# Kernel tuning notes

Hardware: AMD Instinct MI355X
Metric: run time of the kernel (lower is better)

Reference implementation:

```python
import jax, jax.numpy as jnp
import numpy as np

D_MODEL = 1024
D_KEY = 64
BATCH = 4
SEQ = 4096


def setup_inputs() -> dict:
    key = jax.random.key(0)
    kq, kk, kv, kwq, kwk, kwv = jax.random.split(key, 6)
    queries = jax.random.normal(kq, (BATCH, SEQ, D_MODEL), dtype=jnp.float32)
    keys = jax.random.normal(kk, (BATCH, SEQ, D_MODEL), dtype=jnp.float32)
    values = jax.random.normal(kv, (BATCH, SEQ, D_MODEL), dtype=jnp.float32)
    # causal mask: 1 = keep, 0 = masked out (torch masked_fill where mask==0)
    mask = jnp.tril(jnp.ones((SEQ, SEQ), dtype=jnp.int32))
    s = 1.0 / np.sqrt(D_MODEL)
    Wq = jax.random.normal(kwq, (D_MODEL, D_KEY), dtype=jnp.float32) * s
    Wk = jax.random.normal(kwk, (D_MODEL, D_KEY), dtype=jnp.float32) * s
    Wv = jax.random.normal(kwv, (D_MODEL, D_KEY), dtype=jnp.float32) * s
    return {"queries": queries, "keys": keys, "values": values,
            "mask": mask, "Wq": Wq, "Wk": Wk, "Wv": Wv}


def reference(queries, keys, values, mask, Wq, Wk, Wv):
    q = jnp.einsum('bsd,dk->bsk', queries, Wq)   # [B,S,dk]
    k = jnp.einsum('bsd,dk->bsk', keys, Wk)
    v = jnp.einsum('bsd,dk->bsk', values, Wv)
    scale = 1.0 / np.sqrt(D_KEY).astype(np.float32)
    attn = jnp.einsum('bqk,bsk->bqs', q, k) * scale  # [B,Sq,Sk]
    attn = jnp.where(mask == 0, -jnp.inf, attn)
    attn = jax.nn.softmax(attn, axis=-1)
    return jnp.einsum('bqs,bsk->bqk', attn, v)      # [B,S,dk]
```

## Files before the change

kernel.cpp:

```cpp
#include <hip/hip_runtime.h>
#include <hip/hip_bf16.h>

#define B      4
#define SEQ    4096
#define DM     1024
#define DK     64
#define NSPLIT 8

typedef __bf16 bf16x8 __attribute__((ext_vector_type(8)));
typedef __bf16 bf16x4 __attribute__((ext_vector_type(4)));
typedef float  f32x4  __attribute__((ext_vector_type(4)));

#define KSTR 72

#define QSCALE 0.1803368801111204f
#define M2BIAS 12.0f

__global__ __launch_bounds__(256) void wt_kernel(
    const float* __restrict__ Wq, const float* __restrict__ Wk,
    const float* __restrict__ Wv, __bf16* __restrict__ Wt)
{
    const int mat = blockIdx.y;
    const float* W = (mat == 0) ? Wq : (mat == 1) ? Wk : Wv;
    const float scale = (mat == 0) ? QSCALE : 1.0f;
    const int k0 = blockIdx.x * 64;
    const int tid = threadIdx.x;

    __shared__ float t[64][65];

    const int r = tid >> 2;
    const int c = (tid & 3) * 16;
    {
        const float* src = W + (size_t)(k0 + r) * DK + c;
        #pragma unroll
        for (int j = 0; j < 4; ++j) {
            float4 a = *(const float4*)(src + j * 4);
            t[r][c + j * 4 + 0] = a.x; t[r][c + j * 4 + 1] = a.y;
            t[r][c + j * 4 + 2] = a.z; t[r][c + j * 4 + 3] = a.w;
        }
    }
    __syncthreads();
    const int n  = tid >> 2;
    const int kk = (tid & 3) * 16;
    bf16x8 b0, b1;
    #pragma unroll
    for (int j = 0; j < 8; ++j) b0[j] = (__bf16)(t[kk + j][n] * scale);
    #pragma unroll
    for (int j = 0; j < 8; ++j) b1[j] = (__bf16)(t[kk + 8 + j][n] * scale);
    __bf16* dst = Wt + (size_t)(mat * DK + n) * DM + k0 + kk;
    *(bf16x8*)(dst)     = b0;
    *(bf16x8*)(dst + 8) = b1;
}

#define DA 8
#define DW 4
__global__ __launch_bounds__(256) void proj_stream_kernel(
    const float* __restrict__ q_in, const float* __restrict__ k_in,
    const float* __restrict__ v_in, const __bf16* __restrict__ Wt,
    __bf16* __restrict__ qb, __bf16* __restrict__ kb,
    __bf16* __restrict__ vtb)
{
    const int m = blockIdx.y;
    const float* in = (m == 0) ? q_in : (m == 1) ? k_in : v_in;
    const __bf16* wt = Wt + (size_t)m * DK * DM;

    const int rowbase = blockIdx.x * 64;
    const int tid  = threadIdx.x;
    const int w    = tid >> 6;
    const int lane = tid & 63;
    const int quad = lane >> 4;
    const int l15  = lane & 15;

    const float*  arow = in + (size_t)(rowbase + w * 16 + l15) * DM + quad * 8;
    const __bf16* wrow = wt + (size_t)l15 * DM + quad * 8;

    float4 Aa[DA], Ab[DA];
    bf16x8 Wb[DW][4];
    #pragma unroll
    for (int d = 0; d < DA; ++d) {
        const float* ap = arow + d * 32;
        Aa[d] = *(const float4*)(ap);
        Ab[d] = *(const float4*)(ap + 4);
    }
    #pragma unroll
    for (int d = 0; d < DW; ++d) {
        const __bf16* wp = wrow + d * 32;
        Wb[d][0] = *(const bf16x8*)(wp);
        Wb[d][1] = *(const bf16x8*)(wp + 16 * DM);
        Wb[d][2] = *(const bf16x8*)(wp + 32 * DM);
        Wb[d][3] = *(const bf16x8*)(wp + 48 * DM);
    }

    f32x4 acc[4];
    #pragma unroll
    for (int nf = 0; nf < 4; ++nf) acc[nf] = (f32x4){0.f, 0.f, 0.f, 0.f};

    #pragma unroll
    for (int it = 0; it < 32; ++it) {
        const int da = it & (DA - 1);
        const int dw = it & (DW - 1);
        bf16x8 af;
        af[0] = (__bf16)Aa[da].x; af[1] = (__bf16)Aa[da].y;
        af[2] = (__bf16)Aa[da].z; af[3] = (__bf16)Aa[da].w;
        af[4] = (__bf16)Ab[da].x; af[5] = (__bf16)Ab[da].y;
        af[6] = (__bf16)Ab[da].z; af[7] = (__bf16)Ab[da].w;
        acc[0] = __builtin_amdgcn_mfma_f32_16x16x32_bf16(af, Wb[dw][0], acc[0], 0, 0, 0);
        acc[1] = __builtin_amdgcn_mfma_f32_16x16x32_bf16(af, Wb[dw][1], acc[1], 0, 0, 0);
        acc[2] = __builtin_amdgcn_mfma_f32_16x16x32_bf16(af, Wb[dw][2], acc[2], 0, 0, 0);
        acc[3] = __builtin_amdgcn_mfma_f32_16x16x32_bf16(af, Wb[dw][3], acc[3], 0, 0, 0);
        if (it + DA < 32) {
            const float* ap = arow + (it + DA) * 32;
            Aa[da] = *(const float4*)(ap);
            Ab[da] = *(const float4*)(ap + 4);
        }
        if (it + DW < 32) {
            const __bf16* wp = wrow + (it + DW) * 32;
            Wb[dw][0] = *(const bf16x8*)(wp);
            Wb[dw][1] = *(const bf16x8*)(wp + 16 * DM);
            Wb[dw][2] = *(const bf16x8*)(wp + 32 * DM);
            Wb[dw][3] = *(const bf16x8*)(wp + 48 * DM);
        }
    }

    if (m < 2) {
        __bf16* outb = (m == 0) ? qb : kb;
        #pragma unroll
        for (int nf = 0; nf < 4; ++nf)
            #pragma unroll
            for (int r = 0; r < 4; ++r)
                outb[(size_t)(rowbase + w * 16 + quad * 4 + r) * DK + nf * 16 + l15] =
                    (__bf16)acc[nf][r];
    } else {
        const int bb = rowbase >> 12;
        const int s0 = (rowbase & (SEQ - 1)) + w * 16 + quad * 4;
        #pragma unroll
        for (int nf = 0; nf < 4; ++nf) {
            bf16x4 v4;
            #pragma unroll
            for (int r = 0; r < 4; ++r) v4[r] = (__bf16)acc[nf][r];
            *(bf16x4*)&vtb[(size_t)(bb * DK + nf * 16 + l15) * SEQ + s0] = v4;
        }
    }
}

__global__ __launch_bounds__(256) void flash_kernel(
    const __bf16* __restrict__ qb, const __bf16* __restrict__ kb,
    const __bf16* __restrict__ vtb, __bf16* __restrict__ Opart,
    float* __restrict__ lpart)
{
    const int qt  = blockIdx.x;
    const int bb  = blockIdx.y;
    const int z   = blockIdx.z;
    const int tid = threadIdx.x;
    const int w    = tid >> 6;
    const int lane = tid & 63;
    const int quad = lane >> 4;
    const int l15  = lane & 15;

    __shared__ __bf16 Ks[64 * KSTR];
    __shared__ __bf16 Vs[64 * KSTR];
    __shared__ __bf16 Ps[4][2][16 * KSTR];

    const int qrow_base = qt * 128 + w * 32;
    const int niters = 2 * qt + 2;
    const int kt0 = (niters * z) / NSPLIT;
    const int kt1 = (niters * (z + 1)) / NSPLIT;

    bf16x8 qf[2][2];
    #pragma unroll
    for (int g = 0; g < 2; ++g) {
        const __bf16* qp = qb + ((size_t)(bb * SEQ + qrow_base + g * 16 + l15)) * DK + quad * 8;
        qf[g][0] = *(const bf16x8*)(qp);
        qf[g][1] = *(const bf16x8*)(qp + 32);
    }

    bf16x8 ones;
    #pragma unroll
    for (int j = 0; j < 8; ++j) ones[j] = (__bf16)1.0f;

    f32x4 of[2][4], lacc[2];
    #pragma unroll
    for (int g = 0; g < 2; ++g) {
        #pragma unroll
        for (int nf = 0; nf < 4; ++nf) of[g][nf] = (f32x4){0.f, 0.f, 0.f, 0.f};
        lacc[g] = (f32x4){0.f, 0.f, 0.f, 0.f};
    }

    const int sr = tid >> 2;
    const int sc = (tid & 3) * 16;
    bf16x8 kr0, kr1, vr0, vr1;
    const __bf16* kbase = kb  + ((size_t)(bb * SEQ + sr)) * DK + sc;
    const __bf16* vbase = vtb + ((size_t)(bb * DK  + sr)) * SEQ + sc;

    if (kt1 > kt0) {
        const __bf16* kg = kbase + (size_t)kt0 * 64 * DK;
        kr0 = *(const bf16x8*)(kg); kr1 = *(const bf16x8*)(kg + 8);
        const __bf16* vg = vbase + kt0 * 64;
        vr0 = *(const bf16x8*)(vg); vr1 = *(const bf16x8*)(vg + 8);
    }

    for (int kt = kt0; kt < kt1; ++kt) {
        __syncthreads();
        *(bf16x8*)&Ks[sr * KSTR + sc]     = kr0;
        *(bf16x8*)&Ks[sr * KSTR + sc + 8] = kr1;
        *(bf16x8*)&Vs[sr * KSTR + sc]     = vr0;
        *(bf16x8*)&Vs[sr * KSTR + sc + 8] = vr1;
        __syncthreads();
        if (kt + 1 < kt1) {
            const __bf16* kg = kbase + (size_t)(kt + 1) * 64 * DK;
            kr0 = *(const bf16x8*)(kg); kr1 = *(const bf16x8*)(kg + 8);
            const __bf16* vg = vbase + (kt + 1) * 64;
            vr0 = *(const bf16x8*)(vg); vr1 = *(const bf16x8*)(vg + 8);
        }

        f32x4 sf[2][4];
        #pragma unroll
        for (int g = 0; g < 2; ++g)
            #pragma unroll
            for (int nf = 0; nf < 4; ++nf)
                sf[g][nf] = (f32x4){-M2BIAS, -M2BIAS, -M2BIAS, -M2BIAS};
        #pragma unroll
        for (int nf = 0; nf < 4; ++nf) {
            #pragma unroll
            for (int ch = 0; ch < 2; ++ch) {
                bf16x8 kf = *(const bf16x8*)(&Ks[(nf * 16 + l15) * KSTR + ch * 32 + quad * 8]);
                sf[0][nf] = __builtin_amdgcn_mfma_f32_16x16x32_bf16(qf[0][ch], kf, sf[0][nf], 0, 0, 0);
                sf[1][nf] = __builtin_amdgcn_mfma_f32_16x16x32_bf16(qf[1][ch], kf, sf[1][nf], 0, 0, 0);
            }
        }

        const int kc0 = kt * 64;
        #pragma unroll
        for (int g = 0; g < 2; ++g) {
            const int r0 = qrow_base + g * 16;
            const bool dg = (kc0 + 63 > r0);
            #pragma unroll
            for (int nf = 0; nf < 4; ++nf) {
                #pragma unroll
                for (int r = 0; r < 4; ++r) {
                    float s = sf[g][nf][r];
                    if (dg) {
                        const int col = kc0 + nf * 16 + l15;
                        const int row = r0 + quad * 4 + r;
                        if (col > row) s = -1.0e9f;
                    }
                    const float p = __builtin_amdgcn_exp2f(s);
                    Ps[w][g][(quad * 4 + r) * KSTR + nf * 16 + l15] = (__bf16)p;
                }
            }
        }

        bf16x8 pf[2][2];
        #pragma unroll
        for (int g = 0; g < 2; ++g) {
            pf[g][0] = *(const bf16x8*)(&Ps[w][g][l15 * KSTR + quad * 8]);
            pf[g][1] = *(const bf16x8*)(&Ps[w][g][l15 * KSTR + 32 + quad * 8]);
            lacc[g] = __builtin_amdgcn_mfma_f32_16x16x32_bf16(pf[g][0], ones, lacc[g], 0, 0, 0);
            lacc[g] = __builtin_amdgcn_mfma_f32_16x16x32_bf16(pf[g][1], ones, lacc[g], 0, 0, 0);
        }

        #pragma unroll
        for (int nf = 0; nf < 4; ++nf) {
            #pragma unroll
            for (int ch = 0; ch < 2; ++ch) {
                bf16x8 vf = *(const bf16x8*)(&Vs[(nf * 16 + l15) * KSTR + ch * 32 + quad * 8]);
                of[0][nf] = __builtin_amdgcn_mfma_f32_16x16x32_bf16(pf[0][ch], vf, of[0][nf], 0, 0, 0);
                of[1][nf] = __builtin_amdgcn_mfma_f32_16x16x32_bf16(pf[1][ch], vf, of[1][nf], 0, 0, 0);
            }
        }
    }

    #pragma unroll
    for (int g = 0; g < 2; ++g) {
        __bf16* Op = Opart + ((size_t)(z * B + bb) * SEQ + qrow_base + g * 16) * DK;
        #pragma unroll
        for (int nf = 0; nf < 4; ++nf)
            #pragma unroll
            for (int r = 0; r < 4; ++r)
                Op[(size_t)(quad * 4 + r) * DK + nf * 16 + l15] = (__bf16)of[g][nf][r];
        if (l15 == 0) {
            const size_t base = (size_t)(z * B + bb) * SEQ + qrow_base + g * 16 + quad * 4;
            #pragma unroll
            for (int r = 0; r < 4; ++r)
                lpart[base + r] = lacc[g][r];
        }
    }
}

__global__ __launch_bounds__(256) void combine_kernel(
    const __bf16* __restrict__ Opart, const float* __restrict__ lpart,
    float* __restrict__ out)
{
    const int idx = blockIdx.x * 256 + threadIdx.x;
    const int row = idx >> 6;

    float L = 0.f, o = 0.f;
    #pragma unroll
    for (int z = 0; z < NSPLIT; ++z) {
        L += lpart[(size_t)z * (B * SEQ) + row];
        o += (float)Opart[(size_t)z * (B * SEQ) * DK + idx];
    }
    out[idx] = o / L;
}

extern "C" void kernel_launch(void* const* d_in, const int* in_sizes, int n_in,
                              void* d_out, int out_size, void* d_ws, size_t ws_size,
                              hipStream_t stream)
{
    const float* queries = (const float*)d_in[0];
    const float* keys    = (const float*)d_in[1];
    const float* values  = (const float*)d_in[2];
    const float* Wq = (const float*)d_in[4];
    const float* Wk = (const float*)d_in[5];
    const float* Wv = (const float*)d_in[6];
    float* out = (float*)d_out;

    char* p = (char*)d_ws;
    __bf16* qb  = (__bf16*)p;  p += (size_t)B * SEQ * DK * 2;
    __bf16* kb  = (__bf16*)p;  p += (size_t)B * SEQ * DK * 2;
    __bf16* vtb = (__bf16*)p;  p += (size_t)B * SEQ * DK * 2;
    __bf16* Wt  = (__bf16*)p;  p += (size_t)3 * DK * DM * 2;
    __bf16* Opart = (__bf16*)p; p += (size_t)NSPLIT * B * SEQ * DK * 2;
    float* lpart = (float*)p;   p += (size_t)NSPLIT * B * SEQ * 4;

    wt_kernel<<<dim3(DM / 64, 3), 256, 0, stream>>>(Wq, Wk, Wv, Wt);

    proj_stream_kernel<<<dim3((B * SEQ) / 64, 3), 256, 0, stream>>>(
        queries, keys, values, Wt, qb, kb, vtb);

    flash_kernel<<<dim3(SEQ / 128, B, NSPLIT), 256, 0, stream>>>(
        qb, kb, vtb, Opart, lpart);

    combine_kernel<<<(B * SEQ * DK) / 256, 256, 0, stream>>>(
        Opart, lpart, out);
}
```

Before: 297.0 us.

## Stage projection operands through double-buffered LDS with direct global-to-LDS loads

The projection kernel used to stream activation and weight fragments straight into registers, with deep per-thread prefetch queues. It now copies 64x64 tiles of fp32 activations and bf16 weights into double-buffered shared memory using global_load_lds, with XOR swizzling to avoid bank conflicts. MFMA fragments are then read from LDS. This is meant to cut register pressure and make global reads coalesced, at the cost of a barrier per K-chunk and added LDS traffic.

```diff
diff --git a/kernel.cpp b/kernel.cpp
--- a/kernel.cpp
+++ b/kernel.cpp
@@ -16,6 +16,13 @@
 #define QSCALE 0.1803368801111204f
 #define M2BIAS 12.0f
 
+__device__ __forceinline__ void gl_lds16(const void* g, void* l)
+{
+    __builtin_amdgcn_global_load_lds(
+        (const __attribute__((address_space(1))) void*)g,
+        (__attribute__((address_space(3))) void*)l, 16, 0, 0);
+}
+
 __global__ __launch_bounds__(256) void wt_kernel(
     const float* __restrict__ Wq, const float* __restrict__ Wk,
     const float* __restrict__ Wv, __bf16* __restrict__ Wt)
@@ -52,9 +59,7 @@
     *(bf16x8*)(dst + 8) = b1;
 }
 
-#define DA 8
-#define DW 4
-__global__ __launch_bounds__(256) void proj_stream_kernel(
+__global__ __launch_bounds__(256) void proj_lds_kernel(
     const float* __restrict__ q_in, const float* __restrict__ k_in,
     const float* __restrict__ v_in, const __bf16* __restrict__ Wt,
     __bf16* __restrict__ qb, __bf16* __restrict__ kb,
@@ -71,54 +76,66 @@
     const int quad = lane >> 4;
     const int l15  = lane & 15;
 
-    const float*  arow = in + (size_t)(rowbase + w * 16 + l15) * DM + quad * 8;
-    const __bf16* wrow = wt + (size_t)l15 * DM + quad * 8;
-
-    float4 Aa[DA], Ab[DA];
-    bf16x8 Wb[DW][4];
-    #pragma unroll
-    for (int d = 0; d < DA; ++d) {
-        const float* ap = arow + d * 32;
-        Aa[d] = *(const float4*)(ap);
-        Ab[d] = *(const float4*)(ap + 4);
-    }
-    #pragma unroll
-    for (int d = 0; d < DW; ++d) {
-        const __bf16* wp = wrow + d * 32;
-        Wb[d][0] = *(const bf16x8*)(wp);
-        Wb[d][1] = *(const bf16x8*)(wp + 16 * DM);
-        Wb[d][2] = *(const bf16x8*)(wp + 32 * DM);
-        Wb[d][3] = *(const bf16x8*)(wp + 48 * DM);
-    }
+    __shared__ float  As[2][64 * 64];
+    __shared__ __bf16 Ws[2][64 * 64];
+
+    const float* asrc[4];
+    #pragma unroll
+    for (int i = 0; i < 4; ++i) {
+        const int j = w * 4 + i;
+        const int row_local = j * 4 + quad;
+        asrc[i] = in + (size_t)(rowbase + row_local) * DM
+                     + ((l15 ^ (row_local & 7)) << 2);
+    }
+    const __bf16* wsrc[2];
+    const int l8 = lane >> 3, u7 = lane & 7;
+    #pragma unroll
+    for (int i = 0; i < 2; ++i) {
+        const int j2 = w * 2 + i;
+        const int n_local = j2 * 8 + l8;
+        wsrc[i] = wt + (size_t)n_local * DM + ((u7 ^ (n_local & 7)) << 3);
+    }
+
+    auto stage = [&](int b, int c) {
+        #pragma unroll
+        for (int i = 0; i < 4; ++i)
+            gl_lds16(asrc[i] + c * 64, &As[b][(w * 4 + i) * 256]);
+        #pragma unroll
+        for (int i = 0; i < 2; ++i)
+            gl_lds16(wsrc[i] + c * 64, &Ws[b][(w * 2 + i) * 512]);
+    };
 
     f32x4 acc[4];
     #pragma unroll
     for (int nf = 0; nf < 4; ++nf) acc[nf] = (f32x4){0.f, 0.f, 0.f, 0.f};
 
-    #pragma unroll
-    for (int it = 0; it < 32; ++it) {
-        const int da = it & (DA - 1);
-        const int dw = it & (DW - 1);
-        bf16x8 af;
-        af[0] = (__bf16)Aa[da].x; af[1] = (__bf16)Aa[da].y;
-        af[2] = (__bf16)Aa[da].z; af[3] = (__bf16)Aa[da].w;
-        af[4] = (__bf16)Ab[da].x; af[5] = (__bf16)Ab[da].y;
-        af[6] = (__bf16)Ab[da].z; af[7] = (__bf16)Ab[da].w;
-        acc[0] = __builtin_amdgcn_mfma_f32_16x16x32_bf16(af, Wb[dw][0], acc[0], 0, 0, 0);
-        acc[1] = __builtin_amdgcn_mfma_f32_16x16x32_bf16(af, Wb[dw][1], acc[1], 0, 0, 0);
-        acc[2] = __builtin_amdgcn_mfma_f32_16x16x32_bf16(af, Wb[dw][2], acc[2], 0, 0, 0);
-        acc[3] = __builtin_amdgcn_mfma_f32_16x16x32_bf16(af, Wb[dw][3], acc[3], 0, 0, 0);
-        if (it + DA < 32) {
-            const float* ap = arow + (it + DA) * 32;
-            Aa[da] = *(const float4*)(ap);
-            Ab[da] = *(const float4*)(ap + 4);
-        }
-        if (it + DW < 32) {
-            const __bf16* wp = wrow + (it + DW) * 32;
-            Wb[dw][0] = *(const bf16x8*)(wp);
-            Wb[dw][1] = *(const bf16x8*)(wp + 16 * DM);
-            Wb[dw][2] = *(const bf16x8*)(wp + 32 * DM);
-            Wb[dw][3] = *(const bf16x8*)(wp + 48 * DM);
+    stage(0, 0);
+
+    const int row = w * 16 + l15;
+    const int sw7 = l15 & 7;
+
+    for (int c = 0; c < 16; ++c) {
+        __syncthreads();
+        if (c + 1 < 16) stage((c + 1) & 1, c + 1);
+        const int b = c & 1;
+
+        #pragma unroll
+        for (int s = 0; s < 2; ++s) {
+            const int q0 = s * 8 + quad * 2;
+            float4 a0 = *(const float4*)&As[b][row * 64 + (( q0      ^ sw7) << 2)];
+            float4 a1 = *(const float4*)&As[b][row * 64 + (((q0 + 1) ^ sw7) << 2)];
+            bf16x8 af;
+            af[0] = (__bf16)a0.x; af[1] = (__bf16)a0.y;
+            af[2] = (__bf16)a0.z; af[3] = (__bf16)a0.w;
+            af[4] = (__bf16)a1.x; af[5] = (__bf16)a1.y;
+            af[6] = (__bf16)a1.z; af[7] = (__bf16)a1.w;
+            #pragma unroll
+            for (int nf = 0; nf < 4; ++nf) {
+                const int n = nf * 16 + l15;
+                bf16x8 wf = *(const bf16x8*)
+                    &Ws[b][n * 64 + (((s * 4 + quad) ^ sw7) << 3)];
+                acc[nf] = __builtin_amdgcn_mfma_f32_16x16x32_bf16(af, wf, acc[nf], 0, 0, 0);
+            }
         }
     }
 
@@ -325,7 +342,7 @@
 
     wt_kernel<<<dim3(DM / 64, 3), 256, 0, stream>>>(Wq, Wk, Wv, Wt);
 
-    proj_stream_kernel<<<dim3((B * SEQ) / 64, 3), 256, 0, stream>>>(
+    proj_lds_kernel<<<dim3((B * SEQ) / 64, 3), 256, 0, stream>>>(
         queries, keys, values, Wt, qb, kb, vtb);
 
     flash_kernel<<<dim3(SEQ / 128, B, NSPLIT), 256, 0, stream>>>(
```

New measurement: 279.3 us. 6.0% less time.
